# Kernel tuning notes

Hardware: AMD Instinct MI355X
Metric: run time of the kernel (lower is better)

## Reference

```python
import jax, jax.numpy as jnp
import numpy as np

N_SRC = 50000
N_DST = 50000
N_EDGES = 800000
D_IN = 256
NUM_HEADS = 8
OUT_DIM = 16
NEG_SLOPE = 0.2


def setup_inputs() -> dict:
    key = jax.random.key(0)
    ks = jax.random.split(key, 9)
    feat_src = jax.random.normal(ks[0], (N_SRC, D_IN), dtype=jnp.float32)
    feat_dst = jax.random.normal(ks[1], (N_DST, D_IN), dtype=jnp.float32)
    W_src = jax.random.normal(ks[2], (NUM_HEADS * OUT_DIM, D_IN), dtype=jnp.float32) * 0.05
    b_src = jax.random.normal(ks[3], (NUM_HEADS * OUT_DIM,), dtype=jnp.float32) * 0.05
    W_dst = jax.random.normal(ks[4], (NUM_HEADS * OUT_DIM, D_IN), dtype=jnp.float32) * 0.05
    b_dst = jax.random.normal(ks[5], (NUM_HEADS * OUT_DIM,), dtype=jnp.float32) * 0.05
    attn = jax.random.normal(ks[6], (NUM_HEADS, 2 * OUT_DIM), dtype=jnp.float32) * 0.1
    src_idx = jax.random.randint(ks[7], (N_EDGES,), 0, N_SRC, dtype=jnp.int32)
    dst_idx = jax.random.randint(ks[8], (N_EDGES,), 0, N_DST, dtype=jnp.int32)
    return {"feat_src": feat_src, "feat_dst": feat_dst, "W_src": W_src,
            "b_src": b_src, "W_dst": W_dst, "b_dst": b_dst, "attn": attn,
            "src_idx": src_idx, "dst_idx": dst_idx}


def reference(feat_src, feat_dst, W_src, b_src, W_dst, b_dst, attn, src_idx, dst_idx):
    # Node-type-specific linear transforms (feat_drop=0 at inference)
    hs = (feat_src @ W_src.T + b_src).reshape(N_SRC, NUM_HEADS, OUT_DIM)
    hd = (feat_dst @ W_dst.T + b_dst).reshape(N_DST, NUM_HEADS, OUT_DIM)
    # Per-node attention logits: el_i = <hs_i, a_l>, er_j = <hd_j, a_r>
    el = jnp.einsum('nkd,kd->nk', hs, attn[:, :OUT_DIM])  # (N_src, K)
    er = jnp.einsum('nkd,kd->nk', hd, attn[:, OUT_DIM:])  # (N_dst, K)
    # Edge scores: e_uv = LeakyReLU(el_u + er_v)
    e = el[src_idx] + er[dst_idx]                          # (E, K)
    e = jnp.where(e >= 0, e, NEG_SLOPE * e)
    # Edge softmax over incoming edges of each destination node
    m = jax.ops.segment_max(e, dst_idx, num_segments=N_DST)        # (N_dst, K)
    e_exp = jnp.exp(e - m[dst_idx])
    denom = jax.ops.segment_sum(e_exp, dst_idx, num_segments=N_DST)
    a = e_exp / denom[dst_idx]                             # (E, K)
    # Weighted neighbor aggregation: sum_u a_uv * hs_u
    msg = hs[src_idx] * a[:, :, None]                      # (E, K, d_out)
    out = jax.ops.segment_sum(msg, dst_idx, num_segments=N_DST)
    return out.reshape(N_DST, NUM_HEADS * OUT_DIM)
```

## Files before the change

### kernel.cpp

```cpp
#include <hip/hip_runtime.h>
#include <hip/hip_bf16.h>

#define N_SRCC 50000
#define N_DSTC 50000
#define N_EDG 800000
#define NBUK 500
#define DPB 100
#define BCAP 2048
#define EPB 3334
#define NPB 240
#define HSB 196
#define ERB 196

typedef __attribute__((ext_vector_type(8))) short bf16x8;
typedef __attribute__((ext_vector_type(4))) float f32x4;
typedef __attribute__((ext_vector_type(8))) unsigned short us8;

__device__ inline short f2bf(float x) {
  __hip_bfloat16 b = __float2bfloat16(x);
  return *reinterpret_cast<short*>(&b);
}
__device__ inline float bf2f(unsigned hi16) {
  union { unsigned u; float f; } c; c.u = hi16 << 16; return c.f;
}

__global__ void fold_kernel(const float* __restrict__ Wsrc, const float* __restrict__ bsrc,
                            const float* __restrict__ Wdst, const float* __restrict__ bdst,
                            const float* __restrict__ attn,
                            float* __restrict__ U, float* __restrict__ Cc,
                            short* __restrict__ Wbf, short* __restrict__ Ubf,
                            int* __restrict__ bCur) {
  int t = blockIdx.x * blockDim.x + threadIdx.x;
  if (t < 4096) {
    int side = t >> 11;
    int r = (t >> 8) & 7;
    int c = t & 255;
    const float* W = side ? Wdst : Wsrc;
    float s = 0.f;
    #pragma unroll
    for (int d = 0; d < 16; d++)
      s += attn[r*32 + side*16 + d] * W[(r*16 + d)*256 + c];
    U[t] = s;
    if (side == 1) Ubf[r*256 + c] = f2bf(s);
    else           Ubf[2048 + t]  = 0;
    const float4* p = (const float4*)&Wsrc[t*8];
    float4 v0 = p[0], v1 = p[1];
    bf16x8 w;
    w[0]=f2bf(v0.x); w[1]=f2bf(v0.y); w[2]=f2bf(v0.z); w[3]=f2bf(v0.w);
    w[4]=f2bf(v1.x); w[5]=f2bf(v1.y); w[6]=f2bf(v1.z); w[7]=f2bf(v1.w);
    *(bf16x8*)&Wbf[t*8] = w;
  }
  if (t < 16) {
    int side = t >> 3, r = t & 7;
    const float* b = side ? bdst : bsrc;
    float s = 0.f;
    #pragma unroll
    for (int d = 0; d < 16; d++) s += attn[r*32 + side*16 + d] * b[r*16 + d];
    Cc[t] = s;
  }
  if (t < NBUK) bCur[t] = 0;
}

__global__ __launch_bounds__(512) void mega512(
    const float* __restrict__ feat_src, const float* __restrict__ feat_dst,
    const short* __restrict__ Wbf, const short* __restrict__ Ubf,
    const float* __restrict__ bias, const float* __restrict__ attn,
    const float* __restrict__ Cc,
    const int* __restrict__ src, const int* __restrict__ dst,
    int* __restrict__ bCur, unsigned* __restrict__ bData,
    __hip_bfloat16* __restrict__ hsC, float* __restrict__ el,
    float* __restrict__ er) {
  __shared__ __align__(16) char smem[30720];
  int b = blockIdx.x;
  int t = threadIdx.x;

  if (b < NPB) {
    int* h   = (int*)smem;
    int* cur = (int*)(smem + 2048);
    for (int i = t; i < NBUK; i += 512) h[i] = 0;
    __syncthreads();
    int start = b * EPB;
    int end = min(start + EPB, N_EDG);
    for (int e = start + t; e < end; e += 512)
      atomicAdd(&h[dst[e] / DPB], 1);
    __syncthreads();
    for (int i = t; i < NBUK; i += 512) {
      int c = h[i];
      cur[i] = c ? atomicAdd(&bCur[i], c) : 0;
    }
    __syncthreads();
    for (int e = start + t; e < end; e += 512) {
      int d = dst[e], bk = d / DPB;
      int pos = atomicAdd(&cur[bk], 1);
      if (pos < BCAP)
        bData[(size_t)bk*BCAP + pos] = (unsigned)src[e] | ((unsigned)(d - bk*DPB) << 16);
    }
    return;
  }

  if (b < NPB + HSB) {
    short (*As)[40] = (short(*)[40])smem;
    short (*Bs)[40] = (short(*)[40])(smem + 20480);
    int lane = t & 63, wid = t >> 6;
    int wr = wid >> 1, wc = wid & 1;
    int row0 = (b - NPB) * 256;
    int lr = lane & 15, lk = lane >> 4;
    int sr = t >> 1, skq = (t & 1) * 16;
    int br = t >> 2, bq = (t & 3) * 8;
    f32x4 acc[4][4] = {};

    for (int k0 = 0; k0 < 256; k0 += 32) {
      {
        int gr = row0 + sr;
        float4 v0 = {}, v1 = {}, v2 = {}, v3 = {};
        if (gr < N_SRCC) {
          const float4* p = (const float4*)&feat_src[(size_t)gr*256 + k0 + skq];
          v0 = p[0]; v1 = p[1]; v2 = p[2]; v3 = p[3];
        }
        bf16x8 t0, t1;
        t0[0]=f2bf(v0.x); t0[1]=f2bf(v0.y); t0[2]=f2bf(v0.z); t0[3]=f2bf(v0.w);
        t0[4]=f2bf(v1.x); t0[5]=f2bf(v1.y); t0[6]=f2bf(v1.z); t0[7]=f2bf(v1.w);
        t1[0]=f2bf(v2.x); t1[1]=f2bf(v2.y); t1[2]=f2bf(v2.z); t1[3]=f2bf(v2.w);
        t1[4]=f2bf(v3.x); t1[5]=f2bf(v3.y); t1[6]=f2bf(v3.z); t1[7]=f2bf(v3.w);
        *(bf16x8*)&As[sr][skq]     = t0;
        *(bf16x8*)&As[sr][skq + 8] = t1;
      }
      *(bf16x8*)&Bs[br][bq] = *(const bf16x8*)&Wbf[br*256 + k0 + bq];
      __syncthreads();
      bf16x8 af[4], bfr[4];
      #pragma unroll
      for (int m = 0; m < 4; m++)
        af[m] = *(const bf16x8*)&As[wr*64 + m*16 + lr][lk*8];
      #pragma unroll
      for (int n = 0; n < 4; n++)
        bfr[n] = *(const bf16x8*)&Bs[wc*64 + n*16 + lr][lk*8];
      #pragma unroll
      for (int m = 0; m < 4; m++)
        #pragma unroll
        for (int n = 0; n < 4; n++)
          acc[m][n] = __builtin_amdgcn_mfma_f32_16x16x32_bf16(af[m], bfr[n], acc[m][n], 0, 0, 0);
      __syncthreads();
    }
    #pragma unroll
    for (int m = 0; m < 4; m++) {
      int r0 = row0 + wr*64 + m*16 + lk*4;
      #pragma unroll
      for (int n = 0; n < 4; n++) {
        int col = wc*64 + n*16 + lr;
        int h = wc*4 + n;
        float bv = bias[col];
        float al = attn[h*32 + lr];
        #pragma unroll
        for (int j = 0; j < 4; j++) {
          int gr = r0 + j;
          float hv = acc[m][n][j] + bv;
          if (gr < N_SRCC) hsC[(size_t)gr*128 + col] = __float2bfloat16(hv);
          float p = hv * al;
          p += __shfl_xor(p, 1); p += __shfl_xor(p, 2);
          p += __shfl_xor(p, 4); p += __shfl_xor(p, 8);
          if (lr == 0 && gr < N_SRCC) el[gr*8 + h] = p;
        }
      }
    }
    return;
  }

  {
    short (*As)[40]  = (short(*)[40])smem;
    short (*Bu)[264] = (short(*)[264])(smem + 20480);
    int lane = t & 63, w = t >> 6;
    int row0 = (b - NPB - HSB) * 256;
    int lr = lane & 15, lk = lane >> 4;
    int sr = t >> 1, skq = (t & 1) * 16;
    {
      int r = t >> 5, ck = t & 31;
      *(bf16x8*)&Bu[r][ck*8] = *(const bf16x8*)&Ubf[r*256 + ck*8];
    }
    f32x4 acc[2] = {};
    for (int k0 = 0; k0 < 256; k0 += 32) {
      {
        int gr = row0 + sr;
        float4 v0 = {}, v1 = {}, v2 = {}, v3 = {};
        if (gr < N_DSTC) {
          const float4* p = (const float4*)&feat_dst[(size_t)gr*256 + k0 + skq];
          v0 = p[0]; v1 = p[1]; v2 = p[2]; v3 = p[3];
        }
        bf16x8 t0, t1;
        t0[0]=f2bf(v0.x); t0[1]=f2bf(v0.y); t0[2]=f2bf(v0.z); t0[3]=f2bf(v0.w);
        t0[4]=f2bf(v1.x); t0[5]=f2bf(v1.y); t0[6]=f2bf(v1.z); t0[7]=f2bf(v1.w);
        t1[0]=f2bf(v2.x); t1[1]=f2bf(v2.y); t1[2]=f2bf(v2.z); t1[3]=f2bf(v2.w);
        t1[4]=f2bf(v3.x); t1[5]=f2bf(v3.y); t1[6]=f2bf(v3.z); t1[7]=f2bf(v3.w);
        *(bf16x8*)&As[sr][skq]     = t0;
        *(bf16x8*)&As[sr][skq + 8] = t1;
      }
      __syncthreads();
      bf16x8 bu = *(const bf16x8*)&Bu[lr][k0 + lk*8];
      #pragma unroll
      for (int m = 0; m < 2; m++) {
        bf16x8 af = *(const bf16x8*)&As[w*32 + m*16 + lr][lk*8];
        acc[m] = __builtin_amdgcn_mfma_f32_16x16x32_bf16(af, bu, acc[m], 0, 0, 0);
      }
      __syncthreads();
    }
    if (lr < 8) {
      float cb = Cc[8 + lr];
      #pragma unroll
      for (int m = 0; m < 2; m++) {
        int r0 = row0 + w*32 + m*16 + lk*4;
        #pragma unroll
        for (int j = 0; j < 4; j++) {
          int gr2 = r0 + j;
          if (gr2 < N_DSTC) er[gr2*8 + lr] = acc[m][j] + cb;
        }
      }
    }
  }
}

__global__ __launch_bounds__(256) void sort_bucket(const unsigned* __restrict__ bData,
    const int* __restrict__ bCur, int* __restrict__ offS, int* __restrict__ offE,
    unsigned short* __restrict__ srcS) {
  __shared__ int hist[DPB];
  __shared__ int s[128];
  __shared__ int cur[DPB];
  int b = blockIdx.x, t = threadIdx.x;
  int cnt = min(bCur[b], BCAP);
  int base = b * BCAP;
  for (int i = t; i < DPB; i += 256) hist[i] = 0;
  __syncthreads();
  for (int e = t; e < cnt; e += 256) atomicAdd(&hist[bData[base + e] >> 16], 1);
  __syncthreads();
  if (t < 128) s[t] = (t < DPB) ? hist[t] : 0;
  __syncthreads();
  for (int d = 1; d < 128; d <<= 1) {
    int v = (t < 128 && t >= d) ? s[t - d] : 0;
    __syncthreads();
    if (t < 128) s[t] += v;
    __syncthreads();
  }
  if (t < DPB) {
    int excl = s[t] - hist[t];
    cur[t] = excl;
    offS[b * DPB + t] = base + excl;
    offE[b * DPB + t] = base + excl + hist[t];
  }
  __syncthreads();
  for (int e = t; e < cnt; e += 256) {
    unsigned ent = bData[base + e];
    int pos = atomicAdd(&cur[ent >> 16], 1);
    srcS[base + pos] = (unsigned short)(ent & 0xffffu);
  }
}

__global__ __launch_bounds__(256) void aggregate(
    const __hip_bfloat16* __restrict__ hs, const float* __restrict__ el,
    const float* __restrict__ er, const int* __restrict__ offS,
    const int* __restrict__ offE, const unsigned short* __restrict__ srcS,
    float* __restrict__ out) {
  int w = threadIdx.x >> 6;
  int lane = threadIdx.x & 63;
  int jA = blockIdx.x * 8 + w;
  int jB = jA + 4;
  int g = lane >> 4;
  int q = lane & 15;
  int h = q >> 1;
  int e0a = offS[jA], remA = offE[jA] - e0a;
  int e0b = offS[jB], remB = offE[jB] - e0b;
  float erA = er[jA*8 + h];
  float erB = er[jB*8 + h];
  float accA[8] = {}, accB[8] = {};
  float denA = 0.f, denB = 0.f;

  #define AGG_BODY(E, ERH, ACC, DEN) { \
    int s = srcS[E]; \
    float ev = el[s*8 + h] + ERH; \
    ev = ev >= 0.f ? ev : 0.2f * ev; \
    float wg = __expf(ev); \
    DEN += wg; \
    us8 hv = *(const us8*)&hs[(size_t)s*128 + q*8]; \
    _Pragma("unroll") \
    for (int c = 0; c < 8; c++) { \
      ACC[c] = fmaf(wg, bf2f((unsigned)hv[c]), ACC[c]); \
    } \
  }

  int ka = 0, kb = 0;
  while (ka + 8 <= remA && kb + 8 <= remB) {
    AGG_BODY(e0a + ka + g, erA, accA, denA);
    AGG_BODY(e0b + kb + g, erB, accB, denB);
    AGG_BODY(e0a + ka + 4 + g, erA, accA, denA);
    AGG_BODY(e0b + kb + 4 + g, erB, accB, denB);
    ka += 8; kb += 8;
  }
  while (ka + 4 <= remA && kb + 4 <= remB) {
    AGG_BODY(e0a + ka + g, erA, accA, denA);
    AGG_BODY(e0b + kb + g, erB, accB, denB);
    ka += 4; kb += 4;
  }
  while (ka + 4 <= remA) { AGG_BODY(e0a + ka + g, erA, accA, denA); ka += 4; }
  while (kb + 4 <= remB) { AGG_BODY(e0b + kb + g, erB, accB, denB); kb += 4; }
  if (ka + g < remA) AGG_BODY(e0a + ka + g, erA, accA, denA);
  if (kb + g < remB) AGG_BODY(e0b + kb + g, erB, accB, denB);
  #undef AGG_BODY

  #pragma unroll
  for (int c = 0; c < 8; c++) {
    accA[c] += __shfl_xor(accA[c], 16); accA[c] += __shfl_xor(accA[c], 32);
    accB[c] += __shfl_xor(accB[c], 16); accB[c] += __shfl_xor(accB[c], 32);
  }
  denA += __shfl_xor(denA, 16); denA += __shfl_xor(denA, 32);
  denB += __shfl_xor(denB, 16); denB += __shfl_xor(denB, 32);
  if (g == 0) {
    float invA = (remA > 0) ? 1.f / denA : 0.f;
    float invB = (remB > 0) ? 1.f / denB : 0.f;
    float4 r0, r1;
    r0.x = accA[0]*invA; r0.y = accA[1]*invA; r0.z = accA[2]*invA; r0.w = accA[3]*invA;
    r1.x = accA[4]*invA; r1.y = accA[5]*invA; r1.z = accA[6]*invA; r1.w = accA[7]*invA;
    *(float4*)&out[(size_t)jA*128 + q*8]     = r0;
    *(float4*)&out[(size_t)jA*128 + q*8 + 4] = r1;
    r0.x = accB[0]*invB; r0.y = accB[1]*invB; r0.z = accB[2]*invB; r0.w = accB[3]*invB;
    r1.x = accB[4]*invB; r1.y = accB[5]*invB; r1.z = accB[6]*invB; r1.w = accB[7]*invB;
    *(float4*)&out[(size_t)jB*128 + q*8]     = r0;
    *(float4*)&out[(size_t)jB*128 + q*8 + 4] = r1;
  }
}

extern "C" void kernel_launch(void* const* d_in, const int* in_sizes, int n_in,
                              void* d_out, int out_size, void* d_ws, size_t ws_size,
                              hipStream_t stream) {
  const float* feat_src = (const float*)d_in[0];
  const float* feat_dst = (const float*)d_in[1];
  const float* W_src = (const float*)d_in[2];
  const float* b_src = (const float*)d_in[3];
  const float* W_dst = (const float*)d_in[4];
  const float* b_dst = (const float*)d_in[5];
  const float* attn  = (const float*)d_in[6];
  const int* src_idx = (const int*)d_in[7];
  const int* dst_idx = (const int*)d_in[8];
  float* out = (float*)d_out;

  __hip_bfloat16* hs_bf = (__hip_bfloat16*)d_ws;
  float* el = (float*)(hs_bf + (size_t)N_SRCC*128);
  float* er = el + (size_t)N_SRCC*8;
  float* U  = er + (size_t)N_DSTC*8;
  float* Cc = U + 4096;
  short* Wbf = (short*)(Cc + 16);
  short* Ubf = Wbf + 32768;
  int* bCur  = (int*)(Ubf + 4096);
  int* offS  = bCur + NBUK;
  int* offE  = offS + N_DSTC;
  unsigned* bData = (unsigned*)(offE + N_DSTC);
  unsigned short* srcS = (unsigned short*)(bData + (size_t)NBUK*BCAP);

  fold_kernel<<<16, 256, 0, stream>>>(W_src, b_src, W_dst, b_dst, attn, U, Cc, Wbf, Ubf, bCur);
  mega512<<<NPB + HSB + ERB, 512, 0, stream>>>(feat_src, feat_dst, Wbf, Ubf, b_src, attn,
                                               Cc, src_idx, dst_idx, bCur, bData,
                                               hs_bf, el, er);
  sort_bucket<<<NBUK, 256, 0, stream>>>(bData, bCur, offS, offE, srcS);
  aggregate<<<(N_DSTC + 7)/8, 256, 0, stream>>>(hs_bf, el, er, offS, offE, srcS, out);
}
```

Measured before the change: 89.09 us.

## Regroup kernels: fuse fold with edge partitioning, split hs GEMM, fuse er with bucket sort

The weight-folding work and the edge bucketing pass now share one launch, and a memset clears the bucket counters. The hs GEMM gets its own kernel. The er projection runs in the same launch as the per-bucket sort. This changes which stages overlap: fold now runs concurrently with partitioning instead of before it, and the sort runs alongside the er GEMM instead of after the mega kernel. The cost is an extra launch plus the memset, and the hs GEMM no longer overlaps with partitioning.

```diff
diff --git a/kernel.cpp b/kernel.cpp
--- a/kernel.cpp
+++ b/kernel.cpp
@@ -24,152 +24,155 @@
   union { unsigned u; float f; } c; c.u = hi16 << 16; return c.f;
 }
 
-__global__ void fold_kernel(const float* __restrict__ Wsrc, const float* __restrict__ bsrc,
-                            const float* __restrict__ Wdst, const float* __restrict__ bdst,
-                            const float* __restrict__ attn,
-                            float* __restrict__ U, float* __restrict__ Cc,
-                            short* __restrict__ Wbf, short* __restrict__ Ubf,
-                            int* __restrict__ bCur) {
-  int t = blockIdx.x * blockDim.x + threadIdx.x;
-  if (t < 4096) {
-    int side = t >> 11;
-    int r = (t >> 8) & 7;
-    int c = t & 255;
-    const float* W = side ? Wdst : Wsrc;
-    float s = 0.f;
+__global__ __launch_bounds__(512) void foldpart(
+    const float* __restrict__ Wsrc, const float* __restrict__ bsrc,
+    const float* __restrict__ Wdst, const float* __restrict__ bdst,
+    const float* __restrict__ attn,
+    float* __restrict__ U, float* __restrict__ Cc,
+    short* __restrict__ Wbf, short* __restrict__ Ubf,
+    const int* __restrict__ src, const int* __restrict__ dst,
+    int* __restrict__ bCur, unsigned* __restrict__ bData) {
+  __shared__ int h[NBUK];
+  __shared__ int cur[NBUK];
+  int b = blockIdx.x;
+  int tid = threadIdx.x;
+  if (b < 8) {
+    int t = b * 512 + tid;
+    {
+      int side = t >> 11;
+      int r = (t >> 8) & 7;
+      int c = t & 255;
+      const float* W = side ? Wdst : Wsrc;
+      float s = 0.f;
+      #pragma unroll
+      for (int d = 0; d < 16; d++)
+        s += attn[r*32 + side*16 + d] * W[(r*16 + d)*256 + c];
+      U[t] = s;
+      if (side == 1) Ubf[r*256 + c] = f2bf(s);
+      else           Ubf[2048 + t]  = 0;
+      const float4* p = (const float4*)&Wsrc[t*8];
+      float4 v0 = p[0], v1 = p[1];
+      bf16x8 w;
+      w[0]=f2bf(v0.x); w[1]=f2bf(v0.y); w[2]=f2bf(v0.z); w[3]=f2bf(v0.w);
+      w[4]=f2bf(v1.x); w[5]=f2bf(v1.y); w[6]=f2bf(v1.z); w[7]=f2bf(v1.w);
+      *(bf16x8*)&Wbf[t*8] = w;
+    }
+    if (t < 16) {
+      int side = t >> 3, r = t & 7;
+      const float* bb = side ? bdst : bsrc;
+      float s = 0.f;
+      #pragma unroll
+      for (int d = 0; d < 16; d++) s += attn[r*32 + side*16 + d] * bb[r*16 + d];
+      Cc[t] = s;
+    }
+    return;
+  }
+  int pb = b - 8;
+  for (int i = tid; i < NBUK; i += 512) h[i] = 0;
+  __syncthreads();
+  int start = pb * EPB;
+  int end = min(start + EPB, N_EDG);
+  for (int e = start + tid; e < end; e += 512)
+    atomicAdd(&h[dst[e] / DPB], 1);
+  __syncthreads();
+  for (int i = tid; i < NBUK; i += 512) {
+    int c = h[i];
+    cur[i] = c ? atomicAdd(&bCur[i], c) : 0;
+  }
+  __syncthreads();
+  for (int e = start + tid; e < end; e += 512) {
+    int d = dst[e], bk = d / DPB;
+    int pos = atomicAdd(&cur[bk], 1);
+    if (pos < BCAP)
+      bData[(size_t)bk*BCAP + pos] = (unsigned)src[e] | ((unsigned)(d - bk*DPB) << 16);
+  }
+}
+
+__global__ __launch_bounds__(512) void hs512(
+    const float* __restrict__ A, const short* __restrict__ Wbf,
+    const float* __restrict__ bias, const float* __restrict__ attn,
+    __hip_bfloat16* __restrict__ C, float* __restrict__ el) {
+  __shared__ short As[256][40];
+  __shared__ short Bs[128][40];
+  int t = threadIdx.x;
+  int lane = t & 63, wid = t >> 6;
+  int wr = wid >> 1, wc = wid & 1;
+  int row0 = blockIdx.x * 256;
+  int lr = lane & 15, lk = lane >> 4;
+  int sr = t >> 1, skq = (t & 1) * 16;
+  int br = t >> 2, bq = (t & 3) * 8;
+  f32x4 acc[4][4] = {};
+
+  for (int k0 = 0; k0 < 256; k0 += 32) {
+    {
+      int gr = row0 + sr;
+      float4 v0 = {}, v1 = {}, v2 = {}, v3 = {};
+      if (gr < N_SRCC) {
+        const float4* p = (const float4*)&A[(size_t)gr*256 + k0 + skq];
+        v0 = p[0]; v1 = p[1]; v2 = p[2]; v3 = p[3];
+      }
+      bf16x8 t0, t1;
+      t0[0]=f2bf(v0.x); t0[1]=f2bf(v0.y); t0[2]=f2bf(v0.z); t0[3]=f2bf(v0.w);
+      t0[4]=f2bf(v1.x); t0[5]=f2bf(v1.y); t0[6]=f2bf(v1.z); t0[7]=f2bf(v1.w);
+      t1[0]=f2bf(v2.x); t1[1]=f2bf(v2.y); t1[2]=f2bf(v2.z); t1[3]=f2bf(v2.w);
+      t1[4]=f2bf(v3.x); t1[5]=f2bf(v3.y); t1[6]=f2bf(v3.z); t1[7]=f2bf(v3.w);
+      *(bf16x8*)&As[sr][skq]     = t0;
+      *(bf16x8*)&As[sr][skq + 8] = t1;
+    }
+    *(bf16x8*)&Bs[br][bq] = *(const bf16x8*)&Wbf[br*256 + k0 + bq];
+    __syncthreads();
+    bf16x8 af[4], bfr[4];
     #pragma unroll
-    for (int d = 0; d < 16; d++)
-      s += attn[r*32 + side*16 + d] * W[(r*16 + d)*256 + c];
-    U[t] = s;
-    if (side == 1) Ubf[r*256 + c] = f2bf(s);
-    else           Ubf[2048 + t]  = 0;
-    const float4* p = (const float4*)&Wsrc[t*8];
-    float4 v0 = p[0], v1 = p[1];
-    bf16x8 w;
-    w[0]=f2bf(v0.x); w[1]=f2bf(v0.y); w[2]=f2bf(v0.z); w[3]=f2bf(v0.w);
-    w[4]=f2bf(v1.x); w[5]=f2bf(v1.y); w[6]=f2bf(v1.z); w[7]=f2bf(v1.w);
-    *(bf16x8*)&Wbf[t*8] = w;
-  }
-  if (t < 16) {
-    int side = t >> 3, r = t & 7;
-    const float* b = side ? bdst : bsrc;
-    float s = 0.f;
+    for (int m = 0; m < 4; m++)
+      af[m] = *(const bf16x8*)&As[wr*64 + m*16 + lr][lk*8];
     #pragma unroll
-    for (int d = 0; d < 16; d++) s += attn[r*32 + side*16 + d] * b[r*16 + d];
-    Cc[t] = s;
-  }
-  if (t < NBUK) bCur[t] = 0;
-}
-
-__global__ __launch_bounds__(512) void mega512(
-    const float* __restrict__ feat_src, const float* __restrict__ feat_dst,
-    const short* __restrict__ Wbf, const short* __restrict__ Ubf,
-    const float* __restrict__ bias, const float* __restrict__ attn,
-    const float* __restrict__ Cc,
-    const int* __restrict__ src, const int* __restrict__ dst,
-    int* __restrict__ bCur, unsigned* __restrict__ bData,
-    __hip_bfloat16* __restrict__ hsC, float* __restrict__ el,
-    float* __restrict__ er) {
-  __shared__ __align__(16) char smem[30720];
+    for (int n = 0; n < 4; n++)
+      bfr[n] = *(const bf16x8*)&Bs[wc*64 + n*16 + lr][lk*8];
+    #pragma unroll
+    for (int m = 0; m < 4; m++)
+      #pragma unroll
+      for (int n = 0; n < 4; n++)
+        acc[m][n] = __builtin_amdgcn_mfma_f32_16x16x32_bf16(af[m], bfr[n], acc[m][n], 0, 0, 0);
+    __syncthreads();
+  }
+  #pragma unroll
+  for (int m = 0; m < 4; m++) {
+    int r0 = row0 + wr*64 + m*16 + lk*4;
+    #pragma unroll
+    for (int n = 0; n < 4; n++) {
+      int col = wc*64 + n*16 + lr;
+      int h = wc*4 + n;
+      float bv = bias[col];
+      float al = attn[h*32 + lr];
+      #pragma unroll
+      for (int j = 0; j < 4; j++) {
+        int gr = r0 + j;
+        float hv = acc[m][n][j] + bv;
+        if (gr < N_SRCC) C[(size_t)gr*128 + col] = __float2bfloat16(hv);
+        float p = hv * al;
+        p += __shfl_xor(p, 1); p += __shfl_xor(p, 2);
+        p += __shfl_xor(p, 4); p += __shfl_xor(p, 8);
+        if (lr == 0 && gr < N_SRCC) el[gr*8 + h] = p;
+      }
+    }
+  }
+}
+
+__global__ __launch_bounds__(512) void ersort(
+    const float* __restrict__ feat_dst, const short* __restrict__ Ubf,
+    const float* __restrict__ Cc, float* __restrict__ er,
+    const unsigned* __restrict__ bData, const int* __restrict__ bCur,
+    int* __restrict__ offS, int* __restrict__ offE,
+    unsigned short* __restrict__ srcS) {
+  __shared__ __align__(16) char smem[29184];
   int b = blockIdx.x;
   int t = threadIdx.x;
 
-  if (b < NPB) {
-    int* h   = (int*)smem;
-    int* cur = (int*)(smem + 2048);
-    for (int i = t; i < NBUK; i += 512) h[i] = 0;
-    __syncthreads();
-    int start = b * EPB;
-    int end = min(start + EPB, N_EDG);
-    for (int e = start + t; e < end; e += 512)
-      atomicAdd(&h[dst[e] / DPB], 1);
-    __syncthreads();
-    for (int i = t; i < NBUK; i += 512) {
-      int c = h[i];
-      cur[i] = c ? atomicAdd(&bCur[i], c) : 0;
-    }
-    __syncthreads();
-    for (int e = start + t; e < end; e += 512) {
-      int d = dst[e], bk = d / DPB;
-      int pos = atomicAdd(&cur[bk], 1);
-      if (pos < BCAP)
-        bData[(size_t)bk*BCAP + pos] = (unsigned)src[e] | ((unsigned)(d - bk*DPB) << 16);
-    }
-    return;
-  }
-
-  if (b < NPB + HSB) {
-    short (*As)[40] = (short(*)[40])smem;
-    short (*Bs)[40] = (short(*)[40])(smem + 20480);
-    int lane = t & 63, wid = t >> 6;
-    int wr = wid >> 1, wc = wid & 1;
-    int row0 = (b - NPB) * 256;
-    int lr = lane & 15, lk = lane >> 4;
-    int sr = t >> 1, skq = (t & 1) * 16;
-    int br = t >> 2, bq = (t & 3) * 8;
-    f32x4 acc[4][4] = {};
-
-    for (int k0 = 0; k0 < 256; k0 += 32) {
-      {
-        int gr = row0 + sr;
-        float4 v0 = {}, v1 = {}, v2 = {}, v3 = {};
-        if (gr < N_SRCC) {
-          const float4* p = (const float4*)&feat_src[(size_t)gr*256 + k0 + skq];
-          v0 = p[0]; v1 = p[1]; v2 = p[2]; v3 = p[3];
-        }
-        bf16x8 t0, t1;
-        t0[0]=f2bf(v0.x); t0[1]=f2bf(v0.y); t0[2]=f2bf(v0.z); t0[3]=f2bf(v0.w);
-        t0[4]=f2bf(v1.x); t0[5]=f2bf(v1.y); t0[6]=f2bf(v1.z); t0[7]=f2bf(v1.w);
-        t1[0]=f2bf(v2.x); t1[1]=f2bf(v2.y); t1[2]=f2bf(v2.z); t1[3]=f2bf(v2.w);
-        t1[4]=f2bf(v3.x); t1[5]=f2bf(v3.y); t1[6]=f2bf(v3.z); t1[7]=f2bf(v3.w);
-        *(bf16x8*)&As[sr][skq]     = t0;
-        *(bf16x8*)&As[sr][skq + 8] = t1;
-      }
-      *(bf16x8*)&Bs[br][bq] = *(const bf16x8*)&Wbf[br*256 + k0 + bq];
-      __syncthreads();
-      bf16x8 af[4], bfr[4];
-      #pragma unroll
-      for (int m = 0; m < 4; m++)
-        af[m] = *(const bf16x8*)&As[wr*64 + m*16 + lr][lk*8];
-      #pragma unroll
-      for (int n = 0; n < 4; n++)
-        bfr[n] = *(const bf16x8*)&Bs[wc*64 + n*16 + lr][lk*8];
-      #pragma unroll
-      for (int m = 0; m < 4; m++)
-        #pragma unroll
-        for (int n = 0; n < 4; n++)
-          acc[m][n] = __builtin_amdgcn_mfma_f32_16x16x32_bf16(af[m], bfr[n], acc[m][n], 0, 0, 0);
-      __syncthreads();
-    }
-    #pragma unroll
-    for (int m = 0; m < 4; m++) {
-      int r0 = row0 + wr*64 + m*16 + lk*4;
-      #pragma unroll
-      for (int n = 0; n < 4; n++) {
-        int col = wc*64 + n*16 + lr;
-        int h = wc*4 + n;
-        float bv = bias[col];
-        float al = attn[h*32 + lr];
-        #pragma unroll
-        for (int j = 0; j < 4; j++) {
-          int gr = r0 + j;
-          float hv = acc[m][n][j] + bv;
-          if (gr < N_SRCC) hsC[(size_t)gr*128 + col] = __float2bfloat16(hv);
-          float p = hv * al;
-          p += __shfl_xor(p, 1); p += __shfl_xor(p, 2);
-          p += __shfl_xor(p, 4); p += __shfl_xor(p, 8);
-          if (lr == 0 && gr < N_SRCC) el[gr*8 + h] = p;
-        }
-      }
-    }
-    return;
-  }
-
-  {
+  if (b < ERB) {
     short (*As)[40]  = (short(*)[40])smem;
     short (*Bu)[264] = (short(*)[264])(smem + 20480);
     int lane = t & 63, w = t >> 6;
-    int row0 = (b - NPB - HSB) * 256;
+    int row0 = b * 256;
     int lr = lane & 15, lk = lane >> 4;
     int sr = t >> 1, skq = (t & 1) * 16;
     {
@@ -214,41 +217,40 @@
         }
       }
     }
-  }
-}
-
-__global__ __launch_bounds__(256) void sort_bucket(const unsigned* __restrict__ bData,
-    const int* __restrict__ bCur, int* __restrict__ offS, int* __restrict__ offE,
-    unsigned short* __restrict__ srcS) {
-  __shared__ int hist[DPB];
-  __shared__ int s[128];
-  __shared__ int cur[DPB];
-  int b = blockIdx.x, t = threadIdx.x;
-  int cnt = min(bCur[b], BCAP);
-  int base = b * BCAP;
-  for (int i = t; i < DPB; i += 256) hist[i] = 0;
-  __syncthreads();
-  for (int e = t; e < cnt; e += 256) atomicAdd(&hist[bData[base + e] >> 16], 1);
-  __syncthreads();
-  if (t < 128) s[t] = (t < DPB) ? hist[t] : 0;
-  __syncthreads();
-  for (int d = 1; d < 128; d <<= 1) {
-    int v = (t < 128 && t >= d) ? s[t - d] : 0;
-    __syncthreads();
-    if (t < 128) s[t] += v;
-    __syncthreads();
-  }
-  if (t < DPB) {
-    int excl = s[t] - hist[t];
-    cur[t] = excl;
-    offS[b * DPB + t] = base + excl;
-    offE[b * DPB + t] = base + excl + hist[t];
-  }
-  __syncthreads();
-  for (int e = t; e < cnt; e += 256) {
-    unsigned ent = bData[base + e];
-    int pos = atomicAdd(&cur[ent >> 16], 1);
-    srcS[base + pos] = (unsigned short)(ent & 0xffffu);
+    return;
+  }
+
+  {
+    int* hist = (int*)smem;
+    int* s    = hist + DPB;
+    int* cur  = s + 128;
+    int bb = b - ERB;
+    int cnt = min(bCur[bb], BCAP);
+    int base = bb * BCAP;
+    for (int i = t; i < DPB; i += 512) hist[i] = 0;
+    __syncthreads();
+    for (int e = t; e < cnt; e += 512) atomicAdd(&hist[bData[base + e] >> 16], 1);
+    __syncthreads();
+    if (t < 128) s[t] = (t < DPB) ? hist[t] : 0;
+    __syncthreads();
+    for (int d = 1; d < 128; d <<= 1) {
+      int v = (t < 128 && t >= d) ? s[t - d] : 0;
+      __syncthreads();
+      if (t < 128) s[t] += v;
+      __syncthreads();
+    }
+    if (t < DPB) {
+      int excl = s[t] - hist[t];
+      cur[t] = excl;
+      offS[bb * DPB + t] = base + excl;
+      offE[bb * DPB + t] = base + excl + hist[t];
+    }
+    __syncthreads();
+    for (int e = t; e < cnt; e += 512) {
+      unsigned ent = bData[base + e];
+      int pos = atomicAdd(&cur[ent >> 16], 1);
+      srcS[base + pos] = (unsigned short)(ent & 0xffffu);
+    }
   }
 }
 
@@ -352,10 +354,11 @@
   unsigned* bData = (unsigned*)(offE + N_DSTC);
   unsigned short* srcS = (unsigned short*)(bData + (size_t)NBUK*BCAP);
 
-  fold_kernel<<<16, 256, 0, stream>>>(W_src, b_src, W_dst, b_dst, attn, U, Cc, Wbf, Ubf, bCur);
-  mega512<<<NPB + HSB + ERB, 512, 0, stream>>>(feat_src, feat_dst, Wbf, Ubf, b_src, attn,
-                                               Cc, src_idx, dst_idx, bCur, bData,
-                                               hs_bf, el, er);
-  sort_bucket<<<NBUK, 256, 0, stream>>>(bData, bCur, offS, offE, srcS);
+  hipMemsetAsync(bCur, 0, NBUK * sizeof(int), stream);
+  foldpart<<<8 + NPB, 512, 0, stream>>>(W_src, b_src, W_dst, b_dst, attn, U, Cc,
+                                        Wbf, Ubf, src_idx, dst_idx, bCur, bData);
+  hs512<<<HSB, 512, 0, stream>>>(feat_src, Wbf, b_src, attn, hs_bf, el);
+  ersort<<<ERB + NBUK, 512, 0, stream>>>(feat_dst, Ubf, Cc, er,
+                                         bData, bCur, offS, offE, srcS);
   aggregate<<<(N_DSTC + 7)/8, 256, 0, stream>>>(hs_bf, el, er, offS, offE, srcS, out);
 }
```

Measured after the change: 98.23 us. 1.1x slower.
